# Optimization experiments

Hardware: AMD Instinct MI355X
Metric: run time of the kernel (lower is better)

## Reference

```python
import jax, jax.numpy as jnp
import numpy as np

CLASSES = 100
SIGMA = 1.0
K_MIX = 11   # mixup pseudo-label kNN
K_KNN = 3    # knn regularizer


def _pairwise_sq(a, b):
    # ||a_i - b_j||^2 via Gram trick; a:[M,D], b:[N,D] -> [M,N]
    aa = jnp.sum(a * a, axis=1)[:, None]
    bb = jnp.sum(b * b, axis=1)[None, :]
    return aa + bb - 2.0 * (a @ b.T)


def _mode_rows(vals):
    # vals: [M,K] float labels. torch.mode semantics: most frequent value,
    # smallest value on ties.
    eq = vals[:, :, None] == vals[:, None, :]      # [M,K,K]
    counts = jnp.sum(eq.astype(vals.dtype), axis=2)  # [M,K]
    maxc = jnp.max(counts, axis=1, keepdims=True)
    masked = jnp.where(counts == maxc, vals, jnp.inf)
    return jnp.min(masked, axis=1)


def setup_inputs() -> dict:
    key = jax.random.key(0)
    k1, k2, k3, k4 = jax.random.split(key, 4)
    N, D = 4096, 512
    x = jax.random.normal(k1, (N, D), dtype=jnp.float32)
    y = jax.random.randint(k2, (N,), 0, CLASSES).astype(jnp.float32)
    lam = jax.random.beta(k3, 2.0, 2.0, (), dtype=jnp.float32)  # Beta(alpha=2, alpha=2)
    perm = jax.random.permutation(k4, N).astype(jnp.int32)
    return {"x": x, "y": y, "lam": lam, "perm": perm}


def reference(x, y, lam, perm):
    # ---- mixup branch: pseudo-label mixed samples via k=11 NN mode ----
    x_ul = x * lam + x[perm] * (1.0 - lam)              # [N,D]
    d = _pairwise_sq(x_ul, x)                            # [N,N]
    _, idx = jax.lax.top_k(-d, K_MIX)                    # indices of k smallest dists
    y_ul = _mode_rows(y[idx])                            # [N]
    x = jnp.concatenate([x, x_ul], axis=0)               # [2N,D]
    y = jnp.concatenate([y, y_ul], axis=0)               # [2N]

    num = x.shape[0]
    y_int = y.astype(jnp.int32)
    # per-class means (empty classes masked out, as the torch loop skips them)
    counts = jax.ops.segment_sum(jnp.ones((num,), x.dtype), y_int, num_segments=CLASSES)
    mu = jax.ops.segment_sum(x, y_int, num_segments=CLASSES) / jnp.maximum(counts, 1.0)[:, None]
    d2 = _pairwise_sq(x, mu)                             # [num, classes]
    pi = jnp.exp(-d2 / (2.0 * SIGMA ** 2)) * (counts > 0).astype(x.dtype)[None, :]
    yh = jax.nn.one_hot(y_int, CLASSES, dtype=x.dtype)
    eps = 1e-15
    pi = pi / (jnp.sum(pi, axis=1, keepdims=True) + eps)
    pi = jnp.clip(pi, 0.0, 1.0)
    loss_gm = jnp.mean(jnp.sum((pi - yh) ** 2, axis=1))

    # ---- knn regularizer: k=3 NN (excluding self) mode label, MSE ----
    dk = _pairwise_sq(x, x)                              # [num,num]
    _, idxk = jax.lax.top_k(-dk, K_KNN + 1)              # nearest is self (dist 0)
    y_ng = _mode_rows(y[idxk[:, 1:]])
    loss_knn = jnp.mean((y_ng - y) ** 2)
    return loss_gm + 0.01 * loss_knn
```

## Files before the change

kernel.cpp:

```cpp
#include <hip/hip_runtime.h>
#include <math.h>

#define N0   4096
#define D    512
#define NUM  8192
#define NCLS 100
#define KMIX 11

#define OFF_NALL   0
#define OFF_YALL   8192
#define OFF_RLOSS  16384
#define OFF_KSQ    24576
#define OFF_MUSUM  32768
#define OFF_CNT    83968
#define OFF_KNN    84096
#define ZERO_N     51344
#define OFF_NMU    84112
#define OFF_MUT    84224
#define OFF_TK1S   135424
#define OFF_TK1I   659712
#define OFF_TK2S   1184000
#define OFF_TK2I   1446144
#define OFF_XH     1708288
#define TOTAL_F    3805440
#define NEED_BYTES ((size_t)TOTAL_F * 4)

typedef _Float16 half8 __attribute__((ext_vector_type(8)));
typedef _Float16 half4v __attribute__((ext_vector_type(4)));
typedef float f32x4 __attribute__((ext_vector_type(4)));
typedef unsigned long long u64;

__device__ __forceinline__ float4 ld_row4(const float* __restrict__ x, const int* __restrict__ perm,
                                          float lam, float om, int r, int col) {
  if (r < N0) {
    return *(const float4*)(x + (size_t)r * D + col);
  } else {
    int rr = r - N0;
    int p = perm[rr];
    float4 a = *(const float4*)(x + (size_t)rr * D + col);
    float4 b = *(const float4*)(x + (size_t)p * D + col);
    float4 m;
    m.x = lam * a.x + om * b.x;  m.y = lam * a.y + om * b.y;
    m.z = lam * a.z + om * b.z;  m.w = lam * a.w + om * b.w;
    return m;
  }
}

__device__ __forceinline__ void gld_lds16(const _Float16* g, _Float16* l) {
  __builtin_amdgcn_global_load_lds(
      (const __attribute__((address_space(1))) void*)g,
      (__attribute__((address_space(3))) void*)l, 16, 0, 0);
}

__device__ __forceinline__ unsigned sortable(float s) {
  unsigned u = __float_as_uint(s);
  return ((int)u < 0) ? ~u : (u | 0x80000000u);
}
__device__ __forceinline__ float unsortable(unsigned u) {
  return __uint_as_float(((int)u < 0) ? (u & 0x7fffffffu) : ~u);
}

__global__ __launch_bounds__(256) void k_zero(float* __restrict__ p, int n) {
  int i = blockIdx.x * 256 + threadIdx.x;
  if (i < n) p[i] = 0.f;
}

__global__ __launch_bounds__(256) void k_y(const float* __restrict__ y, float* __restrict__ y_all) {
  int i = blockIdx.x * 256 + threadIdx.x;
  if (i < N0) y_all[i] = y[i];
}

__global__ __launch_bounds__(64) void k_prep(const float* __restrict__ x, const float* __restrict__ y,
                                             const int* __restrict__ perm, const float* __restrict__ lam_p,
                                             _Float16* __restrict__ Xh, float* __restrict__ n_all,
                                             float* __restrict__ y_all) {
  int i = blockIdx.x;
  float lam = lam_p[0], om = 1.0f - lam;
  int t = threadIdx.x;
  float4 a = ld_row4(x, perm, lam, om, i, t * 4);
  float4 b = ld_row4(x, perm, lam, om, i, t * 4 + 256);
  half4v ha, hb;
  ha.x = (_Float16)a.x; ha.y = (_Float16)a.y; ha.z = (_Float16)a.z; ha.w = (_Float16)a.w;
  hb.x = (_Float16)b.x; hb.y = (_Float16)b.y; hb.z = (_Float16)b.z; hb.w = (_Float16)b.w;
  *(half4v*)(Xh + (size_t)i * D + t * 4) = ha;
  *(half4v*)(Xh + (size_t)i * D + t * 4 + 256) = hb;
  float s = a.x*a.x + a.y*a.y + a.z*a.z + a.w*a.w
          + b.x*b.x + b.y*b.y + b.z*b.z + b.w*b.w;
  #pragma unroll
  for (int o = 32; o > 0; o >>= 1) s += __shfl_down(s, o, 64);
  if (t == 0) {
    n_all[i] = s;
    if (i < N0) y_all[i] = y[i];
  }
}

template<int M, int NSPL>
__device__ __forceinline__ void knn_body(const _Float16* __restrict__ Xq,
                                         const _Float16* __restrict__ Xc,
                                         const float* __restrict__ nC,
                                         int cb0, int nctiles, int row0, int split,
                                         float* __restrict__ outS, int* __restrict__ outI,
                                         char* smem) {
  _Float16* St = (_Float16*)smem;
  _Float16* Sh = (_Float16*)(smem + 24576);
  u64* Lb = (u64*)smem;

  int tid = threadIdx.x;
  int wave = tid >> 6, lane = tid & 63;
  int wq = wave >> 1, wc = wave & 1;
  int col16 = lane & 15, quad = lane >> 4;

  const _Float16* qg = Xq + (size_t)(wave * 16 + col16) * D + quad * 8;
  int csegA = 2 * wave, csegB = 2 * wave + 1;
  int ldsQ = wave * 1024 + lane * 8;
  int ldsCA = 4096 + csegA * 1024 + lane * 8;
  int ldsCB = 4096 + csegB * 1024 + lane * 8;

  u64 keys[M];
  #pragma unroll
  for (int q = 0; q < M; q++) keys[q] = ~0ULL;

  int r_scan = tid & 63, h_scan = tid >> 6;

  {
    const _Float16* cA = Xc + (size_t)(cb0 + csegA * 16 + col16) * D + quad * 8;
    const _Float16* cB = cA + (size_t)16 * D;
    gld_lds16(qg,      St + ldsQ);  gld_lds16(qg + 32, St + ldsQ + 512);
    gld_lds16(cA,      St + ldsCA); gld_lds16(cA + 32, St + ldsCA + 512);
    gld_lds16(cB,      St + ldsCB); gld_lds16(cB + 32, St + ldsCB + 512);
  }
  __syncthreads();

  for (int ct = 0; ct < nctiles; ct++) {
    int c0 = cb0 + ct * 128;
    const _Float16* cgA = Xc + (size_t)(c0 + csegA * 16 + col16) * D + quad * 8;
    const _Float16* cgB = cgA + (size_t)16 * D;

    f32x4 acc[2][4];
    #pragma unroll
    for (int i = 0; i < 2; i++)
      #pragma unroll
      for (int j = 0; j < 4; j++) acc[i][j] = (f32x4){0.f, 0.f, 0.f, 0.f};

    #pragma unroll
    for (int t = 0; t < 8; t++) {
      const int cur = t & 1;
      if (t < 7) {
        int kk = (t + 1) * 64;
        _Float16* B = St + (cur ^ 1) * 12288;
        gld_lds16(qg + kk,       B + ldsQ);  gld_lds16(qg + kk + 32,  B + ldsQ + 512);
        gld_lds16(cgA + kk,      B + ldsCA); gld_lds16(cgA + kk + 32, B + ldsCA + 512);
        gld_lds16(cgB + kk,      B + ldsCB); gld_lds16(cgB + kk + 32, B + ldsCB + 512);
      } else if (ct + 1 < nctiles) {
        const _Float16* nA = cgA + (size_t)128 * D;
        const _Float16* nB = cgB + (size_t)128 * D;
        gld_lds16(qg,      St + ldsQ);  gld_lds16(qg + 32, St + ldsQ + 512);
        gld_lds16(nA,      St + ldsCA); gld_lds16(nA + 32, St + ldsCA + 512);
        gld_lds16(nB,      St + ldsCB); gld_lds16(nB + 32, St + ldsCB + 512);
      }
      const _Float16* Bc = St + cur * 12288;
      half8 a[2][2], b[4][2];
      #pragma unroll
      for (int i = 0; i < 2; i++)
        #pragma unroll
        for (int h = 0; h < 2; h++)
          a[i][h] = *(const half8*)(Bc + (wq * 2 + i) * 1024 + h * 512 + lane * 8);
      #pragma unroll
      for (int j = 0; j < 4; j++)
        #pragma unroll
        for (int h = 0; h < 2; h++)
          b[j][h] = *(const half8*)(Bc + 4096 + (wc * 4 + j) * 1024 + h * 512 + lane * 8);
      #pragma unroll
      for (int h = 0; h < 2; h++)
        #pragma unroll
        for (int i = 0; i < 2; i++)
          #pragma unroll
          for (int j = 0; j < 4; j++)
            acc[i][j] = __builtin_amdgcn_mfma_f32_16x16x32_f16(a[i][h], b[j][h], acc[i][j], 0, 0, 0);
      __syncthreads();
    }

    #pragma unroll
    for (int j = 0; j < 4; j++) {
      int cl = wc * 64 + j * 16 + col16;
      float ncv = nC[c0 + cl];
      #pragma unroll
      for (int i = 0; i < 2; i++) {
        half4v st;
        st.x = (_Float16)(ncv - 2.f * acc[i][j][0]);
        st.y = (_Float16)(ncv - 2.f * acc[i][j][1]);
        st.z = (_Float16)(ncv - 2.f * acc[i][j][2]);
        st.w = (_Float16)(ncv - 2.f * acc[i][j][3]);
        *(half4v*)&Sh[(size_t)cl * 68 + wq * 32 + i * 16 + quad * 4] = st;
      }
    }
    __syncthreads();

    for (int c = h_scan * 32; c < h_scan * 32 + 32; c++) {
      float s = (float)Sh[c * 68 + r_scan];
      u64 key = ((u64)sortable(s) << 32) | (unsigned)(c0 + c);
      if (key < keys[M - 1]) {
        keys[M - 1] = key;
        #pragma unroll
        for (int p = M - 1; p > 0; p--) {
          if (keys[p] < keys[p - 1]) { u64 tmp = keys[p]; keys[p] = keys[p - 1]; keys[p - 1] = tmp; }
        }
      }
    }
    __syncthreads();
  }

  #pragma unroll
  for (int q = 0; q < M; q++)
    Lb[((size_t)h_scan * 64 + r_scan) * M + q] = keys[q];
  __syncthreads();
  if (tid < 64) {
    int p0 = 0, p1 = 0, p2 = 0, p3 = 0;
    const u64* L0 = Lb + (size_t)(0 * 64 + tid) * M;
    const u64* L1 = Lb + (size_t)(1 * 64 + tid) * M;
    const u64* L2 = Lb + (size_t)(2 * 64 + tid) * M;
    const u64* L3 = Lb + (size_t)(3 * 64 + tid) * M;
    size_t off = (size_t)(row0 + tid) * ((size_t)NSPL * M) + (size_t)split * M;
    #pragma unroll
    for (int q = 0; q < M; q++) {
      u64 k0 = (p0 < M) ? L0[p0] : ~0ULL;
      u64 k1 = (p1 < M) ? L1[p1] : ~0ULL;
      u64 k2 = (p2 < M) ? L2[p2] : ~0ULL;
      u64 k3 = (p3 < M) ? L3[p3] : ~0ULL;
      u64 b01 = k0 < k1 ? k0 : k1;
      u64 b23 = k2 < k3 ? k2 : k3;
      u64 b = b01 < b23 ? b01 : b23;
      if (b == k0) p0++; else if (b == k1) p1++; else if (b == k2) p2++; else p3++;
      outS[off + q] = unsortable((unsigned)(b >> 32));
      outI[off + q] = (int)(unsigned)b;
    }
  }
}

__global__ __launch_bounds__(256, 3) void k_knn_all(const _Float16* __restrict__ Xh,
                                                    const float* __restrict__ n_all,
                                                    float* __restrict__ tk1s, int* __restrict__ tk1i,
                                                    float* __restrict__ tk2s, int* __restrict__ tk2i) {
  __shared__ __align__(16) char smem[49152];
  int bx = blockIdx.x;
  if (bx < 512) {
    int qblk = bx & 127, split = bx >> 7;
    knn_body<8, 4>(Xh + (size_t)(qblk * 64) * D, Xh, n_all,
                   split * 2048, 16, qblk * 64, split, tk2s, tk2i, smem);
  } else {
    int b = bx - 512;
    int qblk = b & 63, split = b >> 6;
    knn_body<16, 8>(Xh + (size_t)(N0 + qblk * 64) * D, Xh, n_all,
                    split * 512, 4, qblk * 64, split, tk1s, tk1i, smem);
  }
}

__global__ __launch_bounds__(256) void k_rr1(const float* __restrict__ x, const int* __restrict__ perm,
                                             const float* __restrict__ lam_p,
                                             const float* __restrict__ tks, const int* __restrict__ tki,
                                             const float* __restrict__ n_all, const float* __restrict__ y,
                                             float* __restrict__ y_all) {
  __shared__ u64 kl[128];
  __shared__ int sidx[16];
  __shared__ float sdot[16];
  int i = blockIdx.x;
  int t = threadIdx.x;
  float lam = lam_p[0], om = 1.f - lam;
  if (t < 128) {
    float s = tks[(size_t)i * 128 + t];
    int id = tki[(size_t)i * 128 + t];
    kl[t] = ((u64)sortable(s) << 32) | (unsigned)id;
  }
  __syncthreads();
  if (t < 128) {
    u64 me = kl[t];
    int rank = 0;
    for (int j = 0; j < 128; j++) rank += (kl[j] < me) ? 1 : 0;
    if (rank < 16) sidx[rank] = (int)(unsigned)me;
  }
  __syncthreads();
  int g = t >> 4, l16 = t & 15;
  int c = sidx[g];
  float dot = 0.f;
  for (int d0 = l16 * 4; d0 < D; d0 += 64) {
    float4 q4 = ld_row4(x, perm, lam, om, N0 + i, d0);
    float4 c4 = *(const float4*)(x + (size_t)c * D + d0);
    dot += q4.x*c4.x + q4.y*c4.y + q4.z*c4.z + q4.w*c4.w;
  }
  #pragma unroll
  for (int o = 8; o > 0; o >>= 1) dot += __shfl_down(dot, o, 16);
  if (l16 == 0) sdot[g] = n_all[c] - 2.f * dot;
  __syncthreads();
  if (t == 0) {
    float es[16]; int ei[16];
    for (int q = 0; q < 16; q++) { es[q] = sdot[q]; ei[q] = sidx[q]; }
    for (int a = 1; a < 16; a++) {
      float s = es[a]; int id = ei[a];
      int b = a - 1;
      while (b >= 0 && (es[b] > s || (es[b] == s && ei[b] > id))) {
        es[b + 1] = es[b]; ei[b + 1] = ei[b]; b--;
      }
      es[b + 1] = s; ei[b + 1] = id;
    }
    float lab[KMIX];
    for (int q = 0; q < KMIX; q++) lab[q] = y[ei[q]];
    float best = 3.0e38f; int bestc = 0;
    for (int q = 0; q < KMIX; q++) {
      int cnt = 0;
      for (int r = 0; r < KMIX; r++) cnt += (lab[r] == lab[q]) ? 1 : 0;
      if (cnt > bestc || (cnt == bestc && lab[q] < best)) { bestc = cnt; best = lab[q]; }
    }
    y_all[N0 + i] = best;
  }
}

__global__ __launch_bounds__(256) void k_rr2(const float* __restrict__ x, const int* __restrict__ perm,
                                             const float* __restrict__ lam_p,
                                             const float* __restrict__ tks, const int* __restrict__ tki,
                                             const float* __restrict__ n_all, const float* __restrict__ y_all,
                                             float* __restrict__ ksq) {
  __shared__ u64 kl[32];
  __shared__ int sidx[8];
  __shared__ float sdot[8];
  int i = blockIdx.x;
  int t = threadIdx.x;
  float lam = lam_p[0], om = 1.f - lam;
  if (t < 32) {
    float s = tks[(size_t)i * 32 + t];
    int id = tki[(size_t)i * 32 + t];
    kl[t] = ((u64)sortable(s) << 32) | (unsigned)id;
  }
  __syncthreads();
  if (t < 32) {
    u64 me = kl[t];
    int rank = 0;
    #pragma unroll
    for (int j = 0; j < 32; j++) rank += (kl[j] < me) ? 1 : 0;
    if (rank < 8) sidx[rank] = (int)(unsigned)me;
  }
  __syncthreads();
  int g = t >> 5, l32 = t & 31;
  int c = sidx[g];
  float dot = 0.f;
  for (int d0 = l32 * 4; d0 < D; d0 += 128) {
    float4 q4 = ld_row4(x, perm, lam, om, i, d0);
    float4 c4 = ld_row4(x, perm, lam, om, c, d0);
    dot += q4.x*c4.x + q4.y*c4.y + q4.z*c4.z + q4.w*c4.w;
  }
  #pragma unroll
  for (int o = 16; o > 0; o >>= 1) dot += __shfl_down(dot, o, 32);
  if (l32 == 0) sdot[g] = n_all[c] - 2.f * dot;
  __syncthreads();
  if (t == 0) {
    float es[8]; int ei[8];
    for (int q = 0; q < 8; q++) { es[q] = sdot[q]; ei[q] = sidx[q]; }
    for (int a = 1; a < 8; a++) {
      float s = es[a]; int id = ei[a];
      int b = a - 1;
      while (b >= 0 && (es[b] > s || (es[b] == s && ei[b] > id))) {
        es[b + 1] = es[b]; ei[b + 1] = ei[b]; b--;
      }
      es[b + 1] = s; ei[b + 1] = id;
    }
    float l1 = y_all[ei[1]], l2 = y_all[ei[2]], l3 = y_all[ei[3]];
    int c1 = 1 + (int)(l2 == l1) + (int)(l3 == l1);
    int c2 = 1 + (int)(l1 == l2) + (int)(l3 == l2);
    int c3 = 1 + (int)(l1 == l3) + (int)(l2 == l3);
    int mc = c1 > c2 ? c1 : c2; mc = mc > c3 ? mc : c3;
    float mv = 3.0e38f;
    if (c1 == mc) mv = fminf(mv, l1);
    if (c2 == mc) mv = fminf(mv, l2);
    if (c3 == mc) mv = fminf(mv, l3);
    float d = mv - y_all[i];
    ksq[i] = d * d;
  }
}

__global__ __launch_bounds__(256) void k_stats2h(const float* __restrict__ x, const int* __restrict__ perm,
                                                 const float* __restrict__ lam_p, const float* __restrict__ y_all,
                                                 _Float16* __restrict__ muH, float* __restrict__ nmu_pad,
                                                 float* __restrict__ counts) {
  __shared__ int cnt;
  __shared__ int lst[NUM];
  __shared__ int lstp[NUM];
  __shared__ float red[256];
  int c = blockIdx.x;
  int t = threadIdx.x;
  if (c >= NCLS) {
    for (int d = t; d < D; d += 256) muH[(size_t)c * D + d] = (_Float16)0.f;
    if (t == 0) { nmu_pad[c] = 0.f; counts[c] = 0.f; }
    return;
  }
  float lam = lam_p[0], om = 1.f - lam;
  float fc = (float)c;
  if (t == 0) cnt = 0;
  __syncthreads();
  for (int i = t; i < NUM; i += 256) {
    if (y_all[i] == fc) {
      int pos = atomicAdd(&cnt, 1);
      lst[pos] = i;
      lstp[pos] = (i >= N0) ? perm[i - N0] : 0;
    }
  }
  __syncthreads();
  int n = cnt;
  float a0 = 0.f, a1 = 0.f;
  for (int m = 0; m < n; m++) {
    int i = lst[m];
    if (i < N0) {
      a0 += x[(size_t)i * D + t];
      a1 += x[(size_t)i * D + t + 256];
    } else {
      int rr = i - N0, p = lstp[m];
      a0 += lam * x[(size_t)rr * D + t] + om * x[(size_t)p * D + t];
      a1 += lam * x[(size_t)rr * D + t + 256] + om * x[(size_t)p * D + t + 256];
    }
  }
  float inv = 1.f / fmaxf((float)n, 1.f);
  float v0 = a0 * inv, v1 = a1 * inv;
  muH[(size_t)c * D + t] = (_Float16)v0;
  muH[(size_t)c * D + t + 256] = (_Float16)v1;
  red[t] = v0 * v0 + v1 * v1;
  __syncthreads();
  for (int o = 128; o > 0; o >>= 1) { if (t < o) red[t] += red[t + o]; __syncthreads(); }
  if (t == 0) { nmu_pad[c] = red[0]; counts[c] = (float)n; }
}

__global__ __launch_bounds__(256) void k_gm2(const _Float16* __restrict__ Xh,
                                             const _Float16* __restrict__ muH,
                                             const float* __restrict__ nmu_pad,
                                             const float* __restrict__ counts,
                                             const float* __restrict__ n_all,
                                             const float* __restrict__ y_all,
                                             float* __restrict__ rloss) {
  __shared__ __align__(16) char smem[49152];
  float* Ss = (float*)smem;
  _Float16* St = (_Float16*)smem;

  int tid = threadIdx.x;
  int wave = tid >> 6, lane = tid & 63;
  int wq = wave >> 1, wc = wave & 1;
  int col16 = lane & 15, quad = lane >> 4;
  int qb = blockIdx.x * 64;

  const _Float16* qg = Xh + (size_t)(qb + wave * 16 + col16) * D + quad * 8;
  int csegA = 2 * wave, csegB = 2 * wave + 1;
  const _Float16* cgA = muH + (size_t)(csegA * 16 + col16) * D + quad * 8;
  const _Float16* cgB = cgA + (size_t)16 * D;
  int ldsQ = wave * 1024 + lane * 8;
  int ldsCA = 4096 + csegA * 1024 + lane * 8;
  int ldsCB = 4096 + csegB * 1024 + lane * 8;

  f32x4 acc[2][4];
  #pragma unroll
  for (int i = 0; i < 2; i++)
    #pragma unroll
    for (int j = 0; j < 4; j++) acc[i][j] = (f32x4){0.f, 0.f, 0.f, 0.f};

  gld_lds16(qg,       St + ldsQ);
  gld_lds16(qg + 32,  St + ldsQ + 512);
  gld_lds16(cgA,      St + ldsCA);
  gld_lds16(cgA + 32, St + ldsCA + 512);
  gld_lds16(cgB,      St + ldsCB);
  gld_lds16(cgB + 32, St + ldsCB + 512);
  __syncthreads();

  #pragma unroll
  for (int t = 0; t < 8; t++) {
    const int cur = t & 1;
    if (t < 7) {
      int kk = (t + 1) * 64;
      _Float16* B = St + (cur ^ 1) * 12288;
      gld_lds16(qg + kk,       B + ldsQ);
      gld_lds16(qg + kk + 32,  B + ldsQ + 512);
      gld_lds16(cgA + kk,      B + ldsCA);
      gld_lds16(cgA + kk + 32, B + ldsCA + 512);
      gld_lds16(cgB + kk,      B + ldsCB);
      gld_lds16(cgB + kk + 32, B + ldsCB + 512);
    }
    const _Float16* Bc = St + cur * 12288;
    half8 a[2][2], b[4][2];
    #pragma unroll
    for (int i = 0; i < 2; i++)
      #pragma unroll
      for (int h = 0; h < 2; h++)
        a[i][h] = *(const half8*)(Bc + (wq * 2 + i) * 1024 + h * 512 + lane * 8);
    #pragma unroll
    for (int j = 0; j < 4; j++)
      #pragma unroll
      for (int h = 0; h < 2; h++)
        b[j][h] = *(const half8*)(Bc + 4096 + (wc * 4 + j) * 1024 + h * 512 + lane * 8);
    #pragma unroll
    for (int h = 0; h < 2; h++)
      #pragma unroll
      for (int i = 0; i < 2; i++)
        #pragma unroll
        for (int j = 0; j < 4; j++)
          acc[i][j] = __builtin_amdgcn_mfma_f32_16x16x32_f16(a[i][h], b[j][h], acc[i][j], 0, 0, 0);
    __syncthreads();
  }

  #pragma unroll
  for (int j = 0; j < 4; j++) {
    int c_local = wc * 64 + j * 16 + col16;
    float ncv = nmu_pad[c_local];
    #pragma unroll
    for (int i = 0; i < 2; i++) {
      float4 st;
      st.x = ncv - 2.f * acc[i][j][0];
      st.y = ncv - 2.f * acc[i][j][1];
      st.z = ncv - 2.f * acc[i][j][2];
      st.w = ncv - 2.f * acc[i][j][3];
      *(float4*)&Ss[(size_t)c_local * 68 + wq * 32 + i * 16 + quad * 4] = st;
    }
  }
  __syncthreads();

  int r = tid & 63, h = tid >> 6;
  float* redm = (float*)(smem + 35840);
  float* mrow = (float*)(smem + 36864);
  float* Sp   = (float*)(smem + 37120);
  float* Ep   = (float*)(smem + 38144);
  float* Yp   = (float*)(smem + 39168);

  float mymin = 3.0e38f;
  for (int c = h * 32; c < h * 32 + 32; c++) {
    if (c < NCLS && counts[c] > 0.f) mymin = fminf(mymin, Ss[c * 68 + r]);
  }
  redm[h * 64 + r] = mymin;
  __syncthreads();
  if (tid < 64) {
    float ms = fminf(fminf(redm[tid], redm[64 + tid]), fminf(redm[128 + tid], redm[192 + tid]));
    mrow[tid] = ms;
  }
  __syncthreads();
  float ms = mrow[r];
  int yc = (int)y_all[qb + r];
  float Sv = 0.f, Se2 = 0.f, ey = 0.f;
  for (int c = h * 32; c < h * 32 + 32; c++) {
    if (c < NCLS && counts[c] > 0.f) {
      float e = expf(-0.5f * (Ss[c * 68 + r] - ms));
      Sv += e; Se2 += e * e;
      if (c == yc) ey = e;
    }
  }
  Sp[h * 64 + r] = Sv; Ep[h * 64 + r] = Se2; Yp[h * 64 + r] = ey;
  __syncthreads();
  if (tid < 64) {
    float S4 = Sp[tid] + Sp[64 + tid] + Sp[128 + tid] + Sp[192 + tid];
    float E4 = Ep[tid] + Ep[64 + tid] + Ep[128 + tid] + Ep[192 + tid];
    float Y4 = Yp[tid] + Yp[64 + tid] + Yp[128 + tid] + Yp[192 + tid];
    float m = n_all[qb + tid] + mrow[tid];
    float E = expf(-0.5f * m);
    float denom = E * S4 + 1e-15f;
    float f = E / denom;
    rloss[qb + tid] = E4 * f * f - 2.f * Y4 * f + 1.f;
  }
}

__global__ __launch_bounds__(256) void k_final_fast(const float* __restrict__ row_loss,
                                                    const float* __restrict__ ksq, float* __restrict__ out) {
  __shared__ float red[256];
  int t = threadIdx.x;
  float s = 0.f;
  for (int i = t; i < NUM; i += 256) s += row_loss[i] + 0.01f * ksq[i];
  red[t] = s;
  __syncthreads();
  for (int o = 128; o > 0; o >>= 1) { if (t < o) red[t] += red[t + o]; __syncthreads(); }
  if (t == 0) out[0] = red[0] / (float)NUM;
}

#define QT 32
#define CTF 128
#define BKF 32

__global__ __launch_bounds__(64) void k_norms(const float* __restrict__ x, const int* __restrict__ perm,
                                              const float* __restrict__ lam_p, float* __restrict__ n_all) {
  int i = blockIdx.x;
  float lam = lam_p[0], om = 1.0f - lam;
  int t = threadIdx.x;
  float4 a = ld_row4(x, perm, lam, om, i, t * 4);
  float4 b = ld_row4(x, perm, lam, om, i, t * 4 + 256);
  float s = a.x*a.x + a.y*a.y + a.z*a.z + a.w*a.w
          + b.x*b.x + b.y*b.y + b.z*b.z + b.w*b.w;
  #pragma unroll
  for (int o = 32; o > 0; o >>= 1) s += __shfl_down(s, o, 64);
  if (t == 0) n_all[i] = s;
}

template<int KK>
__global__ __launch_bounds__(256) void k_knn_f32(const float* __restrict__ x, const int* __restrict__ perm,
                                                 const float* __restrict__ lam_p, int qstart,
                                                 const float* __restrict__ nC, int candPerSplit, int nsplits,
                                                 float* __restrict__ outS, int* __restrict__ outI) {
  __shared__ float Qs[BKF][QT + 4];
  __shared__ float Cs[BKF][CTF + 4];
  __shared__ float Sf[QT][CTF + 4];

  int tid = threadIdx.x;
  float lam = lam_p[0], om = 1.0f - lam;
  int qbase = blockIdx.x * QT;
  int cb = blockIdx.y * candPerSplit;
  int ce = cb + candPerSplit;

  int cx = tid & 31;
  int ry = tid >> 5;
  int lr = tid >> 3;
  int kc = (tid & 7) * 4;

  float ks[KK]; int ki[KK];
  #pragma unroll
  for (int q = 0; q < KK; q++) { ks[q] = 3.0e38f; ki[q] = 0x7fffffff; }

  for (int c0 = cb; c0 < ce; c0 += CTF) {
    float acc[4][4];
    #pragma unroll
    for (int i = 0; i < 4; i++)
      #pragma unroll
      for (int j = 0; j < 4; j++) acc[i][j] = 0.f;

    for (int kk = 0; kk < D; kk += BKF) {
      __syncthreads();
      {
        float4 v = ld_row4(x, perm, lam, om, qstart + qbase + lr, kk + kc);
        Qs[kc + 0][lr] = v.x; Qs[kc + 1][lr] = v.y; Qs[kc + 2][lr] = v.z; Qs[kc + 3][lr] = v.w;
      }
      #pragma unroll
      for (int rr = 0; rr < 4; rr++) {
        int r = lr + rr * 32;
        float4 v = ld_row4(x, perm, lam, om, c0 + r, kk + kc);
        Cs[kc + 0][r] = v.x; Cs[kc + 1][r] = v.y; Cs[kc + 2][r] = v.z; Cs[kc + 3][r] = v.w;
      }
      __syncthreads();
      #pragma unroll
      for (int k = 0; k < BKF; k++) {
        float4 a4 = *(const float4*)&Qs[k][ry * 4];
        float4 b4 = *(const float4*)&Cs[k][cx * 4];
        float av[4] = {a4.x, a4.y, a4.z, a4.w};
        float bv[4] = {b4.x, b4.y, b4.z, b4.w};
        #pragma unroll
        for (int i = 0; i < 4; i++)
          #pragma unroll
          for (int j = 0; j < 4; j++) acc[i][j] += av[i] * bv[j];
      }
    }
    __syncthreads();
    {
      float4 nc4 = *(const float4*)&nC[c0 + cx * 4];
      float ncv[4] = {nc4.x, nc4.y, nc4.z, nc4.w};
      #pragma unroll
      for (int i = 0; i < 4; i++)
        #pragma unroll
        for (int j = 0; j < 4; j++)
          Sf[ry * 4 + i][cx * 4 + j] = ncv[j] - 2.0f * acc[i][j];
    }
    __syncthreads();
    if (tid < QT) {
      for (int c = 0; c < CTF; c++) {
        float s = Sf[tid][c];
        int j = c0 + c;
        bool worse = (s > ks[KK - 1]) || (s == ks[KK - 1] && j > ki[KK - 1]);
        if (!worse) {
          ks[KK - 1] = s; ki[KK - 1] = j;
          #pragma unroll
          for (int p = KK - 1; p > 0; p--) {
            bool sw = (ks[p] < ks[p - 1]) || (ks[p] == ks[p - 1] && ki[p] < ki[p - 1]);
            if (sw) {
              float ts = ks[p]; ks[p] = ks[p - 1]; ks[p - 1] = ts;
              int ti = ki[p]; ki[p] = ki[p - 1]; ki[p - 1] = ti;
            }
          }
        }
      }
    }
  }

  if (tid < QT) {
    int row = qbase + tid;
    size_t off = (size_t)row * (nsplits * KK) + (size_t)blockIdx.y * KK;
    #pragma unroll
    for (int q = 0; q < KK; q++) { outS[off + q] = ks[q]; outI[off + q] = ki[q]; }
  }
}

__global__ __launch_bounds__(256) void k_final1(const float* __restrict__ tks, const int* __restrict__ tki,
                                                const float* __restrict__ y, float* __restrict__ y_all) {
  int i = blockIdx.x * 256 + threadIdx.x;
  if (i >= N0) return;
  const float* sb = tks + (size_t)i * 44;
  const int* ib = tki + (size_t)i * 44;
  int p0 = 0, p1 = 0, p2 = 0, p3 = 0;
  float lab[KMIX];
  #pragma unroll
  for (int q = 0; q < KMIX; q++) {
    float bs = 3.0e38f; int bi = 0x7fffffff; int w = 0;
    if (p0 < 11) { float s = sb[p0];      int id = ib[p0];      if (s < bs || (s == bs && id < bi)) { bs = s; bi = id; w = 0; } }
    if (p1 < 11) { float s = sb[11 + p1]; int id = ib[11 + p1]; if (s < bs || (s == bs && id < bi)) { bs = s; bi = id; w = 1; } }
    if (p2 < 11) { float s = sb[22 + p2]; int id = ib[22 + p2]; if (s < bs || (s == bs && id < bi)) { bs = s; bi = id; w = 2; } }
    if (p3 < 11) { float s = sb[33 + p3]; int id = ib[33 + p3]; if (s < bs || (s == bs && id < bi)) { bs = s; bi = id; w = 3; } }
    if (w == 0) p0++; else if (w == 1) p1++; else if (w == 2) p2++; else p3++;
    lab[q] = y[bi];
  }
  float best = 3.0e38f; int bestc = 0;
  #pragma unroll
  for (int q = 0; q < KMIX; q++) {
    int c = 0;
    #pragma unroll
    for (int r = 0; r < KMIX; r++) c += (lab[r] == lab[q]) ? 1 : 0;
    if (c > bestc || (c == bestc && lab[q] < best)) { bestc = c; best = lab[q]; }
  }
  y_all[N0 + i] = best;
}

__global__ __launch_bounds__(128) void k_stats(const float* __restrict__ x, const int* __restrict__ perm,
                                               const float* __restrict__ lam_p, const float* __restrict__ y_all,
                                               float* __restrict__ mu_sum, float* __restrict__ counts) {
  int i = blockIdx.x;
  float lam = lam_p[0], om = 1.0f - lam;
  int c = (int)y_all[i];
  float* ms = mu_sum + (size_t)c * D;
  int t = threadIdx.x;
  float4 v = ld_row4(x, perm, lam, om, i, t * 4);
  atomicAdd(&ms[t * 4 + 0], v.x);
  atomicAdd(&ms[t * 4 + 1], v.y);
  atomicAdd(&ms[t * 4 + 2], v.z);
  atomicAdd(&ms[t * 4 + 3], v.w);
  if (t == 0) atomicAdd(&counts[c], 1.0f);
}

__global__ __launch_bounds__(256) void k_mufin(const float* __restrict__ mu_sum, const float* __restrict__ counts,
                                               float* __restrict__ muT, float* __restrict__ nmu) {
  __shared__ float red[256];
  int c = blockIdx.x;
  float inv = 1.0f / fmaxf(counts[c], 1.0f);
  int t = threadIdx.x;
  float v0 = mu_sum[(size_t)c * D + t] * inv;
  float v1 = mu_sum[(size_t)c * D + t + 256] * inv;
  muT[(size_t)t * NCLS + c] = v0;
  muT[(size_t)(t + 256) * NCLS + c] = v1;
  red[t] = v0 * v0 + v1 * v1;
  __syncthreads();
  for (int o = 128; o > 0; o >>= 1) { if (t < o) red[t] += red[t + o]; __syncthreads(); }
  if (t == 0) nmu[c] = red[0];
}

__global__ __launch_bounds__(256) void k_final2(const float* __restrict__ t2s, const int* __restrict__ t2i,
                                                const float* __restrict__ y_all, float* __restrict__ knn_acc) {
  __shared__ float red[256];
  int i = blockIdx.x * 256 + threadIdx.x;
  float dd2 = 0.f;
  if (i < NUM) {
    const float* sA = t2s + (size_t)i * 8; const float* sB = sA + 4;
    const int* iA = t2i + (size_t)i * 8;   const int* iB = iA + 4;
    int pa = 0, pb = 0;
    int midx[4];
    #pragma unroll
    for (int q = 0; q < 4; q++) {
      float sa = (pa < 4) ? sA[pa] : 3.0e38f;
      float sb = (pb < 4) ? sB[pb] : 3.0e38f;
      int ia = (pa < 4) ? iA[pa] : 0x7fffffff;
      int ib = (pb < 4) ? iB[pb] : 0x7fffffff;
      bool ta = (sa < sb) || (sa == sb && ia < ib);
      midx[q] = ta ? ia : ib;
      if (ta) pa++; else pb++;
    }
    float l1 = y_all[midx[1]], l2 = y_all[midx[2]], l3 = y_all[midx[3]];
    int c1 = 1 + (int)(l2 == l1) + (int)(l3 == l1);
    int c2 = 1 + (int)(l1 == l2) + (int)(l3 == l2);
    int c3 = 1 + (int)(l1 == l3) + (int)(l2 == l3);
    int mc = c1 > c2 ? c1 : c2; mc = mc > c3 ? mc : c3;
    float mv = 3.0e38f;
    if (c1 == mc) mv = fminf(mv, l1);
    if (c2 == mc) mv = fminf(mv, l2);
    if (c3 == mc) mv = fminf(mv, l3);
    float d = mv - y_all[i];
    dd2 = d * d;
  }
  red[threadIdx.x] = dd2;
  __syncthreads();
  for (int o = 128; o > 0; o >>= 1) { if (threadIdx.x < o) red[threadIdx.x] += red[threadIdx.x + o]; __syncthreads(); }
  if (threadIdx.x == 0) atomicAdd(knn_acc, red[0]);
}

__global__ __launch_bounds__(128) void k_gm(const float* __restrict__ x, const int* __restrict__ perm,
                                            const float* __restrict__ lam_p, const float* __restrict__ y_all,
                                            const float* __restrict__ n_all, const float* __restrict__ muT,
                                            const float* __restrict__ nmu, const float* __restrict__ counts,
                                            float* __restrict__ row_loss) {
  __shared__ float red[128];
  int i = blockIdx.x;
  int t = threadIdx.x;
  float lam = lam_p[0], om = 1.0f - lam;
  bool valid = (t < NCLS) && (counts[t] > 0.f);
  float d2 = 3.0e38f;
  if (t < NCLS) {
    float dot = 0.f;
    for (int d = 0; d < D; d += 4) {
      float4 v = ld_row4(x, perm, lam, om, i, d);
      dot += v.x * muT[(size_t)(d + 0) * NCLS + t];
      dot += v.y * muT[(size_t)(d + 1) * NCLS + t];
      dot += v.z * muT[(size_t)(d + 2) * NCLS + t];
      dot += v.w * muT[(size_t)(d + 3) * NCLS + t];
    }
    d2 = n_all[i] + nmu[t] - 2.f * dot;
  }
  red[t] = valid ? d2 : 3.0e38f;
  __syncthreads();
  for (int o = 64; o > 0; o >>= 1) { if (t < o) red[t] = fminf(red[t], red[t + o]); __syncthreads(); }
  float m = red[0];
  __syncthreads();
  float e = valid ? expf(-0.5f * (d2 - m)) : 0.f;
  red[t] = e;
  __syncthreads();
  for (int o = 64; o > 0; o >>= 1) { if (t < o) red[t] += red[t + o]; __syncthreads(); }
  float S = red[0];
  __syncthreads();
  float E = expf(-0.5f * m);
  float denom = E * S + 1e-15f;
  float pi = e * E / denom;
  pi = fminf(fmaxf(pi, 0.f), 1.f);
  int yc = (int)y_all[i];
  float term = pi * pi - 2.f * ((t == yc) ? pi : 0.f);
  red[t] = valid ? term : 0.f;
  __syncthreads();
  for (int o = 64; o > 0; o >>= 1) { if (t < o) red[t] += red[t + o]; __syncthreads(); }
  if (t == 0) row_loss[i] = red[0] + 1.0f;
}

__global__ __launch_bounds__(256) void k_final_slow(const float* __restrict__ row_loss,
                                                    const float* __restrict__ knn_acc, float* __restrict__ out) {
  __shared__ float red[256];
  int t = threadIdx.x;
  float s = 0.f;
  for (int i = t; i < NUM; i += 256) s += row_loss[i];
  red[t] = s;
  __syncthreads();
  for (int o = 128; o > 0; o >>= 1) { if (t < o) red[t] += red[t + o]; __syncthreads(); }
  if (t == 0) out[0] = red[0] / (float)NUM + 0.01f * (knn_acc[0] / (float)NUM);
}

extern "C" void kernel_launch(void* const* d_in, const int* in_sizes, int n_in,
                              void* d_out, int out_size, void* d_ws, size_t ws_size,
                              hipStream_t stream) {
  const float* x   = (const float*)d_in[0];
  const float* y   = (const float*)d_in[1];
  const float* lam = (const float*)d_in[2];
  const int* perm  = (const int*)d_in[3];
  float* ws = (float*)d_ws;

  float* n_all  = ws + OFF_NALL;
  float* y_all  = ws + OFF_YALL;
  float* rloss  = ws + OFF_RLOSS;
  float* ksq    = ws + OFF_KSQ;
  float* mu_sum = ws + OFF_MUSUM;
  float* counts = ws + OFF_CNT;
  float* knn_acc= ws + OFF_KNN;
  float* nmu    = ws + OFF_NMU;
  float* muT    = ws + OFF_MUT;
  float* tk1s   = ws + OFF_TK1S;
  int*   tk1i   = (int*)(ws + OFF_TK1I);
  float* tk2s   = ws + OFF_TK2S;
  int*   tk2i   = (int*)(ws + OFF_TK2I);
  _Float16* Xh  = (_Float16*)(ws + OFF_XH);
  _Float16* muH = (_Float16*)(ws + OFF_MUSUM);
  float* nmu_pad= ws + OFF_MUT;

  bool fast = ws_size >= NEED_BYTES;

  if (fast) {
    k_prep<<<NUM, 64, 0, stream>>>(x, y, perm, lam, Xh, n_all, y_all);
    k_knn_all<<<1024, 256, 0, stream>>>(Xh, n_all, tk1s, tk1i, tk2s, tk2i);
    k_rr1<<<N0, 256, 0, stream>>>(x, perm, lam, tk1s, tk1i, n_all, y, y_all);
    k_stats2h<<<128, 256, 0, stream>>>(x, perm, lam, y_all, muH, nmu_pad, counts);
    k_rr2<<<NUM, 256, 0, stream>>>(x, perm, lam, tk2s, tk2i, n_all, y_all, ksq);
    k_gm2<<<NUM / 64, 256, 0, stream>>>(Xh, muH, nmu_pad, counts, n_all, y_all, rloss);
    k_final_fast<<<1, 256, 0, stream>>>(rloss, ksq, (float*)d_out);
  } else {
    k_y<<<(N0 + 255) / 256, 256, 0, stream>>>(y, y_all);
    k_zero<<<(ZERO_N + 255) / 256, 256, 0, stream>>>(mu_sum, ZERO_N);
    k_norms<<<NUM, 64, 0, stream>>>(x, perm, lam, n_all);
    dim3 g1(N0 / QT, 4);
    k_knn_f32<KMIX><<<g1, 256, 0, stream>>>(x, perm, lam, N0, n_all, N0 / 4, 4, tk1s, tk1i);
    k_final1<<<(N0 + 255) / 256, 256, 0, stream>>>(tk1s, tk1i, y, y_all);
    k_stats<<<NUM, 128, 0, stream>>>(x, perm, lam, y_all, mu_sum, counts);
    k_mufin<<<NCLS, 256, 0, stream>>>(mu_sum, counts, muT, nmu);
    dim3 g2(NUM / QT, 2);
    k_knn_f32<4><<<g2, 256, 0, stream>>>(x, perm, lam, 0, n_all, NUM / 2, 2, tk2s, tk2i);
    k_final2<<<NUM / 256, 256, 0, stream>>>(tk2s, tk2i, y_all, knn_acc);
    k_gm<<<NUM, 128, 0, stream>>>(x, perm, lam, y_all, n_all, muT, nmu, counts, rloss);
    k_final_slow<<<1, 256, 0, stream>>>(rloss, knn_acc, (float*)d_out);
  }
}
```

Baseline: 633.5 us.

## Hold query fragments in registers for kNN, fuse post kernels and final reduction

The kNN GEMM now keeps the query tile in registers and reads candidate fragments straight from global memory. This removes the LDS double-buffered staging and its per-step barriers, but raises register use, so the occupancy bound drops from 3 to 2. The kNN-regularizer and class-statistics kernels are merged into one launch. The final reduction is folded into the GM kernel with an atomic accumulator and a last-block-done counter, which removes two kernel launches at the cost of a nondeterministic float summation order.

```diff
diff --git a/kernel.cpp b/kernel.cpp
--- a/kernel.cpp
+++ b/kernel.cpp
@@ -73,7 +73,8 @@
 __global__ __launch_bounds__(64) void k_prep(const float* __restrict__ x, const float* __restrict__ y,
                                              const int* __restrict__ perm, const float* __restrict__ lam_p,
                                              _Float16* __restrict__ Xh, float* __restrict__ n_all,
-                                             float* __restrict__ y_all) {
+                                             float* __restrict__ y_all, float* __restrict__ accp,
+                                             int* __restrict__ donep) {
   int i = blockIdx.x;
   float lam = lam_p[0], om = 1.0f - lam;
   int t = threadIdx.x;
@@ -91,6 +92,7 @@
   if (t == 0) {
     n_all[i] = s;
     if (i < N0) y_all[i] = y[i];
+    if (i == 0) { accp[0] = 0.f; donep[0] = 0; }
   }
 }
 
@@ -101,8 +103,7 @@
                                          int cb0, int nctiles, int row0, int split,
                                          float* __restrict__ outS, int* __restrict__ outI,
                                          char* smem) {
-  _Float16* St = (_Float16*)smem;
-  _Float16* Sh = (_Float16*)(smem + 24576);
+  _Float16* Sh = (_Float16*)smem;
   u64* Lb = (u64*)smem;
 
   int tid = threadIdx.x;
@@ -110,31 +111,26 @@
   int wq = wave >> 1, wc = wave & 1;
   int col16 = lane & 15, quad = lane >> 4;
 
-  const _Float16* qg = Xq + (size_t)(wave * 16 + col16) * D + quad * 8;
-  int csegA = 2 * wave, csegB = 2 * wave + 1;
-  int ldsQ = wave * 1024 + lane * 8;
-  int ldsCA = 4096 + csegA * 1024 + lane * 8;
-  int ldsCB = 4096 + csegB * 1024 + lane * 8;
+  const _Float16* q0 = Xq + (size_t)(wq * 32 + col16) * D + quad * 8;
+  const _Float16* q1 = q0 + (size_t)16 * D;
+  half8 aR[8][2][2];
+  #pragma unroll
+  for (int kt = 0; kt < 8; kt++)
+    #pragma unroll
+    for (int h = 0; h < 2; h++) {
+      aR[kt][0][h] = *(const half8*)(q0 + kt * 64 + h * 32);
+      aR[kt][1][h] = *(const half8*)(q1 + kt * 64 + h * 32);
+    }
 
   u64 keys[M];
   #pragma unroll
   for (int q = 0; q < M; q++) keys[q] = ~0ULL;
 
   int r_scan = tid & 63, h_scan = tid >> 6;
-
-  {
-    const _Float16* cA = Xc + (size_t)(cb0 + csegA * 16 + col16) * D + quad * 8;
-    const _Float16* cB = cA + (size_t)16 * D;
-    gld_lds16(qg,      St + ldsQ);  gld_lds16(qg + 32, St + ldsQ + 512);
-    gld_lds16(cA,      St + ldsCA); gld_lds16(cA + 32, St + ldsCA + 512);
-    gld_lds16(cB,      St + ldsCB); gld_lds16(cB + 32, St + ldsCB + 512);
-  }
-  __syncthreads();
 
   for (int ct = 0; ct < nctiles; ct++) {
     int c0 = cb0 + ct * 128;
-    const _Float16* cgA = Xc + (size_t)(c0 + csegA * 16 + col16) * D + quad * 8;
-    const _Float16* cgB = cgA + (size_t)16 * D;
+    const _Float16* bb = Xc + (size_t)(c0 + wc * 64 + col16) * D + quad * 8;
 
     f32x4 acc[2][4];
     #pragma unroll
@@ -143,41 +139,20 @@
       for (int j = 0; j < 4; j++) acc[i][j] = (f32x4){0.f, 0.f, 0.f, 0.f};
 
     #pragma unroll
-    for (int t = 0; t < 8; t++) {
-      const int cur = t & 1;
-      if (t < 7) {
-        int kk = (t + 1) * 64;
-        _Float16* B = St + (cur ^ 1) * 12288;
-        gld_lds16(qg + kk,       B + ldsQ);  gld_lds16(qg + kk + 32,  B + ldsQ + 512);
-        gld_lds16(cgA + kk,      B + ldsCA); gld_lds16(cgA + kk + 32, B + ldsCA + 512);
-        gld_lds16(cgB + kk,      B + ldsCB); gld_lds16(cgB + kk + 32, B + ldsCB + 512);
-      } else if (ct + 1 < nctiles) {
-        const _Float16* nA = cgA + (size_t)128 * D;
-        const _Float16* nB = cgB + (size_t)128 * D;
-        gld_lds16(qg,      St + ldsQ);  gld_lds16(qg + 32, St + ldsQ + 512);
-        gld_lds16(nA,      St + ldsCA); gld_lds16(nA + 32, St + ldsCA + 512);
-        gld_lds16(nB,      St + ldsCB); gld_lds16(nB + 32, St + ldsCB + 512);
-      }
-      const _Float16* Bc = St + cur * 12288;
-      half8 a[2][2], b[4][2];
-      #pragma unroll
-      for (int i = 0; i < 2; i++)
-        #pragma unroll
-        for (int h = 0; h < 2; h++)
-          a[i][h] = *(const half8*)(Bc + (wq * 2 + i) * 1024 + h * 512 + lane * 8);
+    for (int kt = 0; kt < 8; kt++) {
+      half8 b[4][2];
       #pragma unroll
       for (int j = 0; j < 4; j++)
         #pragma unroll
         for (int h = 0; h < 2; h++)
-          b[j][h] = *(const half8*)(Bc + 4096 + (wc * 4 + j) * 1024 + h * 512 + lane * 8);
+          b[j][h] = *(const half8*)(bb + (size_t)(j * 16) * D + kt * 64 + h * 32);
       #pragma unroll
       for (int h = 0; h < 2; h++)
         #pragma unroll
         for (int i = 0; i < 2; i++)
           #pragma unroll
           for (int j = 0; j < 4; j++)
-            acc[i][j] = __builtin_amdgcn_mfma_f32_16x16x32_f16(a[i][h], b[j][h], acc[i][j], 0, 0, 0);
-      __syncthreads();
+            acc[i][j] = __builtin_amdgcn_mfma_f32_16x16x32_f16(aR[kt][i][h], b[j][h], acc[i][j], 0, 0, 0);
     }
 
     #pragma unroll
@@ -237,11 +212,11 @@
   }
 }
 
-__global__ __launch_bounds__(256, 3) void k_knn_all(const _Float16* __restrict__ Xh,
+__global__ __launch_bounds__(256, 2) void k_knn_all(const _Float16* __restrict__ Xh,
                                                     const float* __restrict__ n_all,
                                                     float* __restrict__ tk1s, int* __restrict__ tk1i,
                                                     float* __restrict__ tk2s, int* __restrict__ tk2i) {
-  __shared__ __align__(16) char smem[49152];
+  __shared__ __align__(16) char smem[32768];
   int bx = blockIdx.x;
   if (bx < 512) {
     int qblk = bx & 127, split = bx >> 7;
@@ -314,125 +289,127 @@
   }
 }
 
-__global__ __launch_bounds__(256) void k_rr2(const float* __restrict__ x, const int* __restrict__ perm,
-                                             const float* __restrict__ lam_p,
-                                             const float* __restrict__ tks, const int* __restrict__ tki,
-                                             const float* __restrict__ n_all, const float* __restrict__ y_all,
-                                             float* __restrict__ ksq) {
-  __shared__ u64 kl[32];
-  __shared__ int sidx[8];
-  __shared__ float sdot[8];
-  int i = blockIdx.x;
+__global__ __launch_bounds__(256) void k_post2(const float* __restrict__ x, const int* __restrict__ perm,
+                                               const float* __restrict__ lam_p,
+                                               const float* __restrict__ tks, const int* __restrict__ tki,
+                                               const float* __restrict__ n_all, const float* __restrict__ y_all,
+                                               float* __restrict__ ksq,
+                                               _Float16* __restrict__ muH, float* __restrict__ nmu_pad,
+                                               float* __restrict__ counts) {
+  __shared__ __align__(16) char sm[33824];
+  int bx = blockIdx.x;
   int t = threadIdx.x;
   float lam = lam_p[0], om = 1.f - lam;
-  if (t < 32) {
-    float s = tks[(size_t)i * 32 + t];
-    int id = tki[(size_t)i * 32 + t];
-    kl[t] = ((u64)sortable(s) << 32) | (unsigned)id;
-  }
-  __syncthreads();
-  if (t < 32) {
-    u64 me = kl[t];
-    int rank = 0;
-    #pragma unroll
-    for (int j = 0; j < 32; j++) rank += (kl[j] < me) ? 1 : 0;
-    if (rank < 8) sidx[rank] = (int)(unsigned)me;
-  }
-  __syncthreads();
-  int g = t >> 5, l32 = t & 31;
-  int c = sidx[g];
-  float dot = 0.f;
-  for (int d0 = l32 * 4; d0 < D; d0 += 128) {
-    float4 q4 = ld_row4(x, perm, lam, om, i, d0);
-    float4 c4 = ld_row4(x, perm, lam, om, c, d0);
-    dot += q4.x*c4.x + q4.y*c4.y + q4.z*c4.z + q4.w*c4.w;
-  }
-  #pragma unroll
-  for (int o = 16; o > 0; o >>= 1) dot += __shfl_down(dot, o, 32);
-  if (l32 == 0) sdot[g] = n_all[c] - 2.f * dot;
-  __syncthreads();
-  if (t == 0) {
-    float es[8]; int ei[8];
-    for (int q = 0; q < 8; q++) { es[q] = sdot[q]; ei[q] = sidx[q]; }
-    for (int a = 1; a < 8; a++) {
-      float s = es[a]; int id = ei[a];
-      int b = a - 1;
-      while (b >= 0 && (es[b] > s || (es[b] == s && ei[b] > id))) {
-        es[b + 1] = es[b]; ei[b + 1] = ei[b]; b--;
-      }
-      es[b + 1] = s; ei[b + 1] = id;
-    }
-    float l1 = y_all[ei[1]], l2 = y_all[ei[2]], l3 = y_all[ei[3]];
-    int c1 = 1 + (int)(l2 == l1) + (int)(l3 == l1);
-    int c2 = 1 + (int)(l1 == l2) + (int)(l3 == l2);
-    int c3 = 1 + (int)(l1 == l3) + (int)(l2 == l3);
-    int mc = c1 > c2 ? c1 : c2; mc = mc > c3 ? mc : c3;
-    float mv = 3.0e38f;
-    if (c1 == mc) mv = fminf(mv, l1);
-    if (c2 == mc) mv = fminf(mv, l2);
-    if (c3 == mc) mv = fminf(mv, l3);
-    float d = mv - y_all[i];
-    ksq[i] = d * d;
-  }
-}
-
-__global__ __launch_bounds__(256) void k_stats2h(const float* __restrict__ x, const int* __restrict__ perm,
-                                                 const float* __restrict__ lam_p, const float* __restrict__ y_all,
-                                                 _Float16* __restrict__ muH, float* __restrict__ nmu_pad,
-                                                 float* __restrict__ counts) {
-  __shared__ int cnt;
-  __shared__ int lst[NUM];
-  __shared__ int lstp[NUM];
-  __shared__ float red[256];
-  int c = blockIdx.x;
-  int t = threadIdx.x;
-  if (c >= NCLS) {
-    for (int d = t; d < D; d += 256) muH[(size_t)c * D + d] = (_Float16)0.f;
-    if (t == 0) { nmu_pad[c] = 0.f; counts[c] = 0.f; }
-    return;
-  }
-  float lam = lam_p[0], om = 1.f - lam;
-  float fc = (float)c;
-  if (t == 0) cnt = 0;
-  __syncthreads();
-  for (int i = t; i < NUM; i += 256) {
-    if (y_all[i] == fc) {
-      int pos = atomicAdd(&cnt, 1);
-      lst[pos] = i;
-      lstp[pos] = (i >= N0) ? perm[i - N0] : 0;
-    }
-  }
-  __syncthreads();
-  int n = cnt;
-  float a0 = 0.f, a1 = 0.f;
-  for (int m = 0; m < n; m++) {
-    int i = lst[m];
-    if (i < N0) {
-      a0 += x[(size_t)i * D + t];
-      a1 += x[(size_t)i * D + t + 256];
-    } else {
-      int rr = i - N0, p = lstp[m];
-      a0 += lam * x[(size_t)rr * D + t] + om * x[(size_t)p * D + t];
-      a1 += lam * x[(size_t)rr * D + t + 256] + om * x[(size_t)p * D + t + 256];
-    }
-  }
-  float inv = 1.f / fmaxf((float)n, 1.f);
-  float v0 = a0 * inv, v1 = a1 * inv;
-  muH[(size_t)c * D + t] = (_Float16)v0;
-  muH[(size_t)c * D + t + 256] = (_Float16)v1;
-  red[t] = v0 * v0 + v1 * v1;
-  __syncthreads();
-  for (int o = 128; o > 0; o >>= 1) { if (t < o) red[t] += red[t + o]; __syncthreads(); }
-  if (t == 0) { nmu_pad[c] = red[0]; counts[c] = (float)n; }
-}
-
-__global__ __launch_bounds__(256) void k_gm2(const _Float16* __restrict__ Xh,
-                                             const _Float16* __restrict__ muH,
-                                             const float* __restrict__ nmu_pad,
-                                             const float* __restrict__ counts,
-                                             const float* __restrict__ n_all,
-                                             const float* __restrict__ y_all,
-                                             float* __restrict__ rloss) {
+
+  if (bx < NUM) {
+    u64* kl = (u64*)sm;
+    int* sidx = (int*)(sm + 256);
+    float* sdot = (float*)(sm + 288);
+    int i = bx;
+    if (t < 32) {
+      float s = tks[(size_t)i * 32 + t];
+      int id = tki[(size_t)i * 32 + t];
+      kl[t] = ((u64)sortable(s) << 32) | (unsigned)id;
+    }
+    __syncthreads();
+    if (t < 32) {
+      u64 me = kl[t];
+      int rank = 0;
+      #pragma unroll
+      for (int j = 0; j < 32; j++) rank += (kl[j] < me) ? 1 : 0;
+      if (rank < 8) sidx[rank] = (int)(unsigned)me;
+    }
+    __syncthreads();
+    int g = t >> 5, l32 = t & 31;
+    int c = sidx[g];
+    float dot = 0.f;
+    for (int d0 = l32 * 4; d0 < D; d0 += 128) {
+      float4 q4 = ld_row4(x, perm, lam, om, i, d0);
+      float4 c4 = ld_row4(x, perm, lam, om, c, d0);
+      dot += q4.x*c4.x + q4.y*c4.y + q4.z*c4.z + q4.w*c4.w;
+    }
+    #pragma unroll
+    for (int o = 16; o > 0; o >>= 1) dot += __shfl_down(dot, o, 32);
+    if (l32 == 0) sdot[g] = n_all[c] - 2.f * dot;
+    __syncthreads();
+    if (t == 0) {
+      float es[8]; int ei[8];
+      for (int q = 0; q < 8; q++) { es[q] = sdot[q]; ei[q] = sidx[q]; }
+      for (int a = 1; a < 8; a++) {
+        float s = es[a]; int id = ei[a];
+        int b = a - 1;
+        while (b >= 0 && (es[b] > s || (es[b] == s && ei[b] > id))) {
+          es[b + 1] = es[b]; ei[b + 1] = ei[b]; b--;
+        }
+        es[b + 1] = s; ei[b + 1] = id;
+      }
+      float l1 = y_all[ei[1]], l2 = y_all[ei[2]], l3 = y_all[ei[3]];
+      int c1 = 1 + (int)(l2 == l1) + (int)(l3 == l1);
+      int c2 = 1 + (int)(l1 == l2) + (int)(l3 == l2);
+      int c3 = 1 + (int)(l1 == l3) + (int)(l2 == l3);
+      int mc = c1 > c2 ? c1 : c2; mc = mc > c3 ? mc : c3;
+      float mv = 3.0e38f;
+      if (c1 == mc) mv = fminf(mv, l1);
+      if (c2 == mc) mv = fminf(mv, l2);
+      if (c3 == mc) mv = fminf(mv, l3);
+      float d = mv - y_all[i];
+      ksq[i] = d * d;
+    }
+  } else {
+    int c = bx - NUM;
+    int* lst = (int*)sm;
+    float* red = (float*)(sm + 32768);
+    int* cntp = (int*)(sm + 33792);
+    if (c >= NCLS) {
+      for (int d = t; d < D; d += 256) muH[(size_t)c * D + d] = (_Float16)0.f;
+      if (t == 0) { nmu_pad[c] = 0.f; counts[c] = 0.f; }
+      return;
+    }
+    float fc = (float)c;
+    if (t == 0) cntp[0] = 0;
+    __syncthreads();
+    for (int i = t; i < NUM; i += 256) {
+      if (y_all[i] == fc) {
+        int pos = atomicAdd(cntp, 1);
+        int p = (i >= N0) ? perm[i - N0] : 0;
+        lst[pos] = i | (p << 13);
+      }
+    }
+    __syncthreads();
+    int n = cntp[0];
+    float a0 = 0.f, a1 = 0.f;
+    for (int m = 0; m < n; m++) {
+      int v = lst[m];
+      int i = v & 8191;
+      if (i < N0) {
+        a0 += x[(size_t)i * D + t];
+        a1 += x[(size_t)i * D + t + 256];
+      } else {
+        int rr = i - N0, p = v >> 13;
+        a0 += lam * x[(size_t)rr * D + t] + om * x[(size_t)p * D + t];
+        a1 += lam * x[(size_t)rr * D + t + 256] + om * x[(size_t)p * D + t + 256];
+      }
+    }
+    float inv = 1.f / fmaxf((float)n, 1.f);
+    float v0 = a0 * inv, v1 = a1 * inv;
+    muH[(size_t)c * D + t] = (_Float16)v0;
+    muH[(size_t)c * D + t + 256] = (_Float16)v1;
+    red[t] = v0 * v0 + v1 * v1;
+    __syncthreads();
+    for (int o = 128; o > 0; o >>= 1) { if (t < o) red[t] += red[t + o]; __syncthreads(); }
+    if (t == 0) { nmu_pad[c] = red[0]; counts[c] = (float)n; }
+  }
+}
+
+__global__ __launch_bounds__(256) void k_gm2f(const _Float16* __restrict__ Xh,
+                                              const _Float16* __restrict__ muH,
+                                              const float* __restrict__ nmu_pad,
+                                              const float* __restrict__ counts,
+                                              const float* __restrict__ n_all,
+                                              const float* __restrict__ y_all,
+                                              const float* __restrict__ ksq,
+                                              float* __restrict__ accp, int* __restrict__ donep,
+                                              float* __restrict__ out) {
   __shared__ __align__(16) char smem[49152];
   float* Ss = (float*)smem;
   _Float16* St = (_Float16*)smem;
@@ -522,6 +499,7 @@
   float* Sp   = (float*)(smem + 37120);
   float* Ep   = (float*)(smem + 38144);
   float* Yp   = (float*)(smem + 39168);
+  float* Rf   = (float*)(smem + 40192);
 
   float mymin = 3.0e38f;
   for (int c = h * 32; c < h * 32 + 32; c++) {
@@ -554,20 +532,21 @@
     float E = expf(-0.5f * m);
     float denom = E * S4 + 1e-15f;
     float f = E / denom;
-    rloss[qb + tid] = E4 * f * f - 2.f * Y4 * f + 1.f;
-  }
-}
-
-__global__ __launch_bounds__(256) void k_final_fast(const float* __restrict__ row_loss,
-                                                    const float* __restrict__ ksq, float* __restrict__ out) {
-  __shared__ float red[256];
-  int t = threadIdx.x;
-  float s = 0.f;
-  for (int i = t; i < NUM; i += 256) s += row_loss[i] + 0.01f * ksq[i];
-  red[t] = s;
-  __syncthreads();
-  for (int o = 128; o > 0; o >>= 1) { if (t < o) red[t] += red[t + o]; __syncthreads(); }
-  if (t == 0) out[0] = red[0] / (float)NUM;
+    float row = E4 * f * f - 2.f * Y4 * f + 1.f + 0.01f * ksq[qb + tid];
+    #pragma unroll
+    for (int o = 32; o > 0; o >>= 1) row += __shfl_down(row, o, 64);
+    Rf[tid] = row;
+  }
+  __syncthreads();
+  if (tid == 0) {
+    atomicAdd(accp, Rf[0]);
+    __threadfence();
+    int old = atomicAdd(donep, 1);
+    if (old == (int)gridDim.x - 1) {
+      float v = atomicAdd(accp, 0.0f);
+      out[0] = v / (float)NUM;
+    }
+  }
 }
 
 #define QT 32
@@ -864,17 +843,19 @@
   _Float16* Xh  = (_Float16*)(ws + OFF_XH);
   _Float16* muH = (_Float16*)(ws + OFF_MUSUM);
   float* nmu_pad= ws + OFF_MUT;
+  float* accp   = ws + OFF_KNN;
+  int*   donep  = (int*)(ws + OFF_KNN + 1);
 
   bool fast = ws_size >= NEED_BYTES;
 
   if (fast) {
-    k_prep<<<NUM, 64, 0, stream>>>(x, y, perm, lam, Xh, n_all, y_all);
+    k_prep<<<NUM, 64, 0, stream>>>(x, y, perm, lam, Xh, n_all, y_all, accp, donep);
     k_knn_all<<<1024, 256, 0, stream>>>(Xh, n_all, tk1s, tk1i, tk2s, tk2i);
     k_rr1<<<N0, 256, 0, stream>>>(x, perm, lam, tk1s, tk1i, n_all, y, y_all);
-    k_stats2h<<<128, 256, 0, stream>>>(x, perm, lam, y_all, muH, nmu_pad, counts);
-    k_rr2<<<NUM, 256, 0, stream>>>(x, perm, lam, tk2s, tk2i, n_all, y_all, ksq);
-    k_gm2<<<NUM / 64, 256, 0, stream>>>(Xh, muH, nmu_pad, counts, n_all, y_all, rloss);
-    k_final_fast<<<1, 256, 0, stream>>>(rloss, ksq, (float*)d_out);
+    k_post2<<<NUM + 128, 256, 0, stream>>>(x, perm, lam, tk2s, tk2i, n_all, y_all,
+                                           ksq, muH, nmu_pad, counts);
+    k_gm2f<<<NUM / 64, 256, 0, stream>>>(Xh, muH, nmu_pad, counts, n_all, y_all,
+                                         ksq, accp, donep, (float*)d_out);
   } else {
     k_y<<<(N0 + 255) / 256, 256, 0, stream>>>(y, y_all);
     k_zero<<<(ZERO_N + 255) / 256, 256, 0, stream>>>(mu_sum, ZERO_N);
```

Result: slower. 783.3 us (+23.6%).
